# Kernel tuning notes

Measured on AMD Instinct MI355X. Metric: run time of the kernel, lower is better.

The kernel has to match this reference:

```python
import jax, jax.numpy as jnp
import numpy as np

DT = 0.001  # seconds per step (keras_spiking default)
BATCH, SEQ, SIZE = 64, 1024, 512


def setup_inputs() -> dict:
    key = jax.random.key(0)
    k1, k2 = jax.random.split(key)
    inputs = jax.random.normal(k1, (BATCH, SEQ, SIZE), dtype=jnp.float32)
    initial_level = jnp.zeros((SIZE,), dtype=jnp.float32)
    # time constants around the 0.01s used in the docstring example
    tau = 0.005 + 0.05 * jax.random.uniform(k2, (SIZE,), dtype=jnp.float32)
    return {"inputs": inputs, "initial_level": initial_level, "tau": tau}


def _alpha_filter(inputs, initial_level, tau):
    # inputs: [B, T, K]; initial_level, tau: [K]
    B_, T, K = inputs.shape
    tau_c = jnp.maximum(tau, 1e-8)               # clip for stability (as in forward pass)
    dt_tau = DT / tau_c                           # [K]
    dt_tau2 = dt_tau / tau_c                      # [K]
    e = jnp.exp(-dt_tau)                          # [K]
    # per-feature 2x2 transition matrix A: [K, 2, 2]
    row0 = jnp.stack([1.0 - dt_tau, -dt_tau2], axis=-1)             # [K, 2]
    row1 = jnp.stack([DT * jnp.ones_like(tau_c), 1.0 + dt_tau], -1)  # [K, 2]
    A = e[:, None, None] * jnp.stack([row0, row1], axis=-2)          # [K, 2, 2]
    # input vector B: [K, 2]
    Bvec = jnp.stack([e * dt_tau2, 1.0 - e * (1.0 + dt_tau)], axis=-1)
    Bt = Bvec.T  # [2, K]
    # initial state: row 0 zeros, row 1 initial_level -> [B, 2, K]
    x0 = jnp.stack(
        [jnp.zeros((B_, K), inputs.dtype),
         jnp.broadcast_to(initial_level, (B_, K))], axis=1)

    def step(x, u):
        # x: [B, 2, K], u: [B, K]
        xn = jnp.einsum('kij,mjk->mik', A, x) + Bt[None, :, :] * u[:, None, :]
        return xn, xn[:, 1]  # output is second state component

    _, ys = jax.lax.scan(step, x0, jnp.swapaxes(inputs, 0, 1))  # ys: [T, B, K]
    return jnp.swapaxes(ys, 0, 1)  # [B, T, K]


def reference(inputs, initial_level, tau):
    return _alpha_filter(inputs, initial_level, tau)
```

## Files before the change

### kernel.cpp

```cpp
#include <hip/hip_runtime.h>
#include <math.h>

namespace {
constexpr int kB = 64;
constexpr int kT = 1024;
constexpr int kK = 512;
constexpr int kP = 32;
constexpr float kDT = 0.001f;
}

__global__ __launch_bounds__(64, 1) void alpha_scan(
    const float* __restrict__ in,
    const float* __restrict__ init_level,
    const float* __restrict__ tau,
    float* __restrict__ out)
{
    const int gid = blockIdx.x * blockDim.x + threadIdx.x;
    const int k = gid & (kK - 1);
    const int b = gid >> 9;

    const float tc      = fmaxf(tau[k], 1e-8f);
    const float dt_tau  = kDT / tc;
    const float dt_tau2 = dt_tau / tc;
    const float e       = expf(-dt_tau);

    const float a00 = e * (1.0f - dt_tau);
    const float a01 = e * (-dt_tau2);
    const float a10 = e * kDT;
    const float a11 = e * (1.0f + dt_tau);
    const float b0  = e * dt_tau2;
    const float b1  = 1.0f - e * (1.0f + dt_tau);

    float x0 = 0.0f;
    float x1 = init_level[k];

    const float* __restrict__ pin = in  + (size_t)b * kT * kK + k;
    float* __restrict__ pout      = out + (size_t)b * kT * kK + k;

    float buf[kP];
    #pragma unroll
    for (int i = 0; i < kP; ++i) buf[i] = pin[(size_t)i * kK];

    for (int tb = 0; tb < kT - kP; tb += kP) {
        const float* __restrict__ pld = pin  + (size_t)(tb + kP) * kK;
        float* __restrict__ pst       = pout + (size_t)tb * kK;
        #pragma unroll
        for (int i = 0; i < kP; ++i) {
            const float u = buf[i];
            buf[i] = pld[(size_t)i * kK];
            const float nx0 = fmaf(a00, x0, fmaf(a01, x1, b0 * u));
            const float nx1 = fmaf(a10, x0, fmaf(a11, x1, b1 * u));
            x0 = nx0; x1 = nx1;
            pst[(size_t)i * kK] = nx1;
        }
    }
    {
        float* __restrict__ pst = pout + (size_t)(kT - kP) * kK;
        #pragma unroll
        for (int i = 0; i < kP; ++i) {
            const float u = buf[i];
            const float nx0 = fmaf(a00, x0, fmaf(a01, x1, b0 * u));
            const float nx1 = fmaf(a10, x0, fmaf(a11, x1, b1 * u));
            x0 = nx0; x1 = nx1;
            pst[(size_t)i * kK] = nx1;
        }
    }
}

extern "C" void kernel_launch(void* const* d_in, const int* in_sizes, int n_in,
                              void* d_out, int out_size, void* d_ws, size_t ws_size,
                              hipStream_t stream) {
    const float* in  = (const float*)d_in[0];
    const float* il  = (const float*)d_in[1];
    const float* tau = (const float*)d_in[2];
    float* out = (float*)d_out;

    const int total = kB * kK;
    dim3 block(64);
    dim3 grid(total / 64);
    alpha_scan<<<grid, block, 0, stream>>>(in, il, tau, out);
}
```

Baseline: 236.9 us.

## Split time axis into chunks with parallel scan and carry propagation

Replaces the one-thread-per-(batch,feature) sequential scan over 1024 steps with a chunked scan. Each of 16 threads per feature scans a 64-step chunk from zero state, chunk end states are exchanged through shared memory, and A^64 is used to propagate carries before a correction pass adds the homogeneous response. This exposes much more parallelism than the original 512 wavefronts, in exchange for extra arithmetic, 64 registers of buffering per thread, and reordered floating-point accumulation.

```diff
diff --git a/kernel.cpp b/kernel.cpp
--- a/kernel.cpp
+++ b/kernel.cpp
@@ -2,22 +2,31 @@
 #include <math.h>
 
 namespace {
-constexpr int kB = 64;
-constexpr int kT = 1024;
-constexpr int kK = 512;
-constexpr int kP = 32;
+constexpr int kB  = 64;
+constexpr int kT  = 1024;
+constexpr int kK  = 512;
+constexpr int kC  = 16;
+constexpr int kL  = kT / kC;
+constexpr int kKB = 32;
+constexpr int kBlockThreads = kKB * kC;
 constexpr float kDT = 0.001f;
 }
 
-__global__ __launch_bounds__(64, 1) void alpha_scan(
+__global__ __launch_bounds__(kBlockThreads, 4) void alpha_scan_chunked(
     const float* __restrict__ in,
     const float* __restrict__ init_level,
     const float* __restrict__ tau,
     float* __restrict__ out)
 {
-    const int gid = blockIdx.x * blockDim.x + threadIdx.x;
-    const int k = gid & (kK - 1);
-    const int b = gid >> 9;
+    __shared__ float sx0[kC][kKB];
+    __shared__ float sx1[kC][kKB];
+
+    const int tid = threadIdx.x;
+    const int kl  = tid & (kKB - 1);
+    const int c   = tid >> 5;
+    const int bx  = blockIdx.x;
+    const int b   = bx >> 4;
+    const int k   = ((bx & 15) << 5) + kl;
 
     const float tc      = fmaxf(tau[k], 1e-8f);
     const float dt_tau  = kDT / tc;
@@ -31,39 +40,51 @@
     const float b0  = e * dt_tau2;
     const float b1  = 1.0f - e * (1.0f + dt_tau);
 
-    float x0 = 0.0f;
-    float x1 = init_level[k];
+    const size_t base = (size_t)b * kT * kK + (size_t)c * kL * kK + k;
+    const float* __restrict__ pin  = in  + base;
+    float* __restrict__ pout       = out + base;
 
-    const float* __restrict__ pin = in  + (size_t)b * kT * kK + k;
-    float* __restrict__ pout      = out + (size_t)b * kT * kK + k;
+    float r[kL];
+    #pragma unroll
+    for (int i = 0; i < kL; ++i) r[i] = pin[(size_t)i * kK];
 
-    float buf[kP];
+    float x0 = 0.0f, x1 = 0.0f;
     #pragma unroll
-    for (int i = 0; i < kP; ++i) buf[i] = pin[(size_t)i * kK];
+    for (int i = 0; i < kL; ++i) {
+        const float u   = r[i];
+        const float nx0 = fmaf(a00, x0, fmaf(a01, x1, b0 * u));
+        const float nx1 = fmaf(a10, x0, fmaf(a11, x1, b1 * u));
+        x0 = nx0; x1 = nx1;
+        r[i] = nx1;
+    }
 
-    for (int tb = 0; tb < kT - kP; tb += kP) {
-        const float* __restrict__ pld = pin  + (size_t)(tb + kP) * kK;
-        float* __restrict__ pst       = pout + (size_t)tb * kK;
-        #pragma unroll
-        for (int i = 0; i < kP; ++i) {
-            const float u = buf[i];
-            buf[i] = pld[(size_t)i * kK];
-            const float nx0 = fmaf(a00, x0, fmaf(a01, x1, b0 * u));
-            const float nx1 = fmaf(a10, x0, fmaf(a11, x1, b1 * u));
-            x0 = nx0; x1 = nx1;
-            pst[(size_t)i * kK] = nx1;
-        }
+    sx0[c][kl] = x0;
+    sx1[c][kl] = x1;
+    __syncthreads();
+
+    float m00 = a00, m01 = a01, m10 = a10, m11 = a11;
+    #pragma unroll
+    for (int s = 0; s < 6; ++s) {
+        const float t00 = fmaf(m00, m00, m01 * m10);
+        const float t01 = fmaf(m00, m01, m01 * m11);
+        const float t10 = fmaf(m10, m00, m11 * m10);
+        const float t11 = fmaf(m10, m01, m11 * m11);
+        m00 = t00; m01 = t01; m10 = t10; m11 = t11;
     }
-    {
-        float* __restrict__ pst = pout + (size_t)(kT - kP) * kK;
-        #pragma unroll
-        for (int i = 0; i < kP; ++i) {
-            const float u = buf[i];
-            const float nx0 = fmaf(a00, x0, fmaf(a01, x1, b0 * u));
-            const float nx1 = fmaf(a10, x0, fmaf(a11, x1, b1 * u));
-            x0 = nx0; x1 = nx1;
-            pst[(size_t)i * kK] = nx1;
-        }
+
+    float v0 = 0.0f, v1 = init_level[k];
+    for (int j = 0; j < c; ++j) {
+        const float p0 = fmaf(m00, v0, m01 * v1) + sx0[j][kl];
+        const float p1 = fmaf(m10, v0, m11 * v1) + sx1[j][kl];
+        v0 = p0; v1 = p1;
+    }
+
+    #pragma unroll
+    for (int i = 0; i < kL; ++i) {
+        const float n0 = fmaf(a00, v0, a01 * v1);
+        const float n1 = fmaf(a10, v0, a11 * v1);
+        v0 = n0; v1 = n1;
+        pout[(size_t)i * kK] = r[i] + n1;
     }
 }
 
@@ -75,8 +96,7 @@
     const float* tau = (const float*)d_in[2];
     float* out = (float*)d_out;
 
-    const int total = kB * kK;
-    dim3 block(64);
-    dim3 grid(total / 64);
-    alpha_scan<<<grid, block, 0, stream>>>(in, il, tau, out);
+    dim3 block(kBlockThreads);
+    dim3 grid(kB * (kK / kKB));
+    alpha_scan_chunked<<<grid, block, 0, stream>>>(in, il, tau, out);
 }
```

Result: slower. 246.7 us (+4.1%).
